# Kernel optimization log

Measured on AMD Instinct MI355X. Metric: run time of the kernel, lower is better.

## Reference

```python
import jax, jax.numpy as jnp
import numpy as np

B = 1024      # batch
HG = 28       # grid side (28x28 image -> graph)
N = HG * HG   # 784 nodes per sample
K = 70        # node_sampled (relaxed categorical classes)
GCN_OUT = 48
H_DIM = 400
Z = 70
IMG = 784
TEMP = 0.5


def _grid_edges():
    idx = np.arange(N).reshape(HG, HG)
    src = np.concatenate([idx[:, :-1].ravel(), idx[:, 1:].ravel(), idx[:-1, :].ravel(), idx[1:, :].ravel()])
    dst = np.concatenate([idx[:, 1:].ravel(), idx[:, :-1].ravel(), idx[1:, :].ravel(), idx[:-1, :].ravel()])
    loop = np.arange(N)
    return (np.concatenate([src, loop]).astype(np.int32),
            np.concatenate([dst, loop]).astype(np.int32))


def _lin(key, fi, fo):
    kw, kb = jax.random.split(key)
    s = 1.0 / np.sqrt(fi)
    return (jax.random.uniform(kw, (fi, fo), jnp.float32, -s, s),
            jax.random.uniform(kb, (fo,), jnp.float32, -s, s))


def setup_inputs() -> dict:
    key = jax.random.key(0)
    ks = jax.random.split(key, 16)
    src, dst = _grid_edges()
    u = jax.random.uniform(ks[2], (B, N, K), jnp.float32, 1e-6, 1.0 - 1e-6)
    inp = {
        'nodes': jax.random.normal(ks[0], (B, N, 2), jnp.float32),
        'logits': jax.random.normal(ks[1], (B, N, K), jnp.float32),
        'gumbel': -jnp.log(-jnp.log(u)),
        'eps': jax.random.normal(ks[3], (B, Z), jnp.float32),
    }
    inp['W1'], inp['b1'] = _lin(ks[4], 2, 16)
    inp['W2'], inp['b2'] = _lin(ks[5], 16, 32)
    inp['W3'], inp['b3'] = _lin(ks[6], 32, GCN_OUT)
    inp['We1'], inp['be1'] = _lin(ks[7], K * GCN_OUT, H_DIM)
    inp['We2'], inp['be2'] = _lin(ks[8], H_DIM, H_DIM)
    inp['Wmu'], inp['bmu'] = _lin(ks[9], H_DIM, Z)
    inp['Wvar'], inp['bvar'] = _lin(ks[10], H_DIM, Z)
    inp['Wd1'], inp['bd1'] = _lin(ks[11], Z, H_DIM)
    inp['Wd2'], inp['bd2'] = _lin(ks[12], H_DIM, IMG)
    inp['edge_src'] = jnp.asarray(src)
    inp['edge_dst'] = jnp.asarray(dst)
    return inp


def reference(nodes, logits, gumbel, eps,
              W1, b1, W2, b2, W3, b3,
              We1, be1, We2, be2,
              Wmu, bmu, Wvar, bvar,
              Wd1, bd1, Wd2, bd2,
              edge_src, edge_dst):
    # symmetric GCN normalization with self loops (already in edge list)
    deg = jnp.zeros((N,), nodes.dtype).at[edge_dst].add(1.0)
    dinv = jax.lax.rsqrt(deg)
    norm = dinv[edge_src] * dinv[edge_dst]  # [E]

    def gcn(h, W, b):
        h = h @ W                                   # [B,N,Fout]
        msg = h[:, edge_src] * norm[None, :, None]  # gather + scale, [B,E,Fout]
        return jnp.zeros_like(h).at[:, edge_dst].add(msg) + b

    h = jax.nn.relu(gcn(nodes, W1, b1))
    h = jax.nn.relu(gcn(h, W2, b2))
    h = jax.nn.relu(gcn(h, W3, b3))            # [B,N,48]

    # RelaxedOneHotCategorical(temp=0.5).rsample() == gumbel-softmax
    sample = jax.nn.softmax((logits + gumbel) / TEMP, axis=-1)  # [B,N,K]
    g = jnp.einsum('bnk,bnf->bkf', sample, h).reshape(h.shape[0], K * GCN_OUT)

    # encoder MLP + reparameterize
    e = jax.nn.relu(g @ We1 + be1)
    e = jax.nn.relu(e @ We2 + be2)
    mu = e @ Wmu + bmu
    var = jax.nn.softplus(e @ Wvar + bvar)
    z = mu + eps * jnp.sqrt(var + 1e-10)

    # decoder
    d = jax.nn.relu(z @ Wd1 + bd1)
    x_rec = jax.nn.sigmoid(d @ Wd2 + bd2)      # [B,784]
    return x_rec
```

## Files before the change

kernel.cpp:

```cpp
#include <hip/hip_runtime.h>
#include <hip/hip_bf16.h>


#define BB 1024
#define HG 28
#define NN 784
#define KK 70
#define F3 48
#define HD 400
#define ZD 70
#define IMGD 784

typedef __hip_bfloat16 bf16;
typedef __attribute__((ext_vector_type(8))) short s8v;
typedef __attribute__((ext_vector_type(4))) float f32x4;

__device__ __forceinline__ float dinv_ij(int i, int j){
  int deg = 1 + (i>0) + (i<HG-1) + (j>0) + (j<HG-1);
  return rsqrtf((float)deg);
}

__device__ __forceinline__ unsigned pk2(float a, float b){
  union { bf16 h; unsigned short u; } ua, ub;
  ua.h = __float2bfloat16(a); ub.h = __float2bfloat16(b);
  return ((unsigned)ub.u << 16) | ua.u;
}

__device__ __forceinline__ short bfbits(float v){
  union { bf16 h; short s; } u; u.h = __float2bfloat16(v); return u.s;
}

#define SYNC_LDS() do {                                   \
    asm volatile("" ::: "memory");                        \
    asm volatile("s_waitcnt lgkmcnt(0)" ::: "memory");    \
    __builtin_amdgcn_s_barrier();                         \
    asm volatile("" ::: "memory");                        \
  } while(0)

__global__ __launch_bounds__(256, 2)
void gcn_fused(const float* __restrict__ nodes,
               const float* __restrict__ W1, const float* __restrict__ b1,
               const float* __restrict__ W2, const float* __restrict__ b2,
               const float* __restrict__ W3, const float* __restrict__ b3,
               bf16* __restrict__ h3){
  __shared__ __align__(16) char smem[73216];
  float* regA = (float*)smem;
  float* regB = (float*)(smem + 36288);
  float* wbuf = (float*)(smem + 64512);
  float* W1s = wbuf;          float* b1s = wbuf + 32;
  float* W2s = wbuf + 48;     float* b2s = wbuf + 560;
  float* W3s = wbuf + 592;    float* b3s = wbuf + 2128;

  int tid = threadIdx.x;
  if (tid < 32)  W1s[tid] = W1[tid];
  if (tid < 16)  b1s[tid] = b1[tid];
  for (int t = tid; t < 512;  t += 256) W2s[t] = W2[t];
  if (tid < 32)  b2s[tid] = b2[tid];
  for (int t = tid; t < 1536; t += 256) W3s[t] = W3[t];
  if (tid < 48)  b3s[tid] = b3[tid];

  int b = blockIdx.x >> 2, s = blockIdx.x & 3;
  int base3 = s*7;
  int base2 = base3 - 1;
  int base1 = base3 - 2;
  const float* nb = nodes + (size_t)b*NN*2;
  __syncthreads();

  {
    float* h1s = regA;
    for (int t = tid; t < 308; t += 256){
      int lr = t/28, j = t - lr*28;
      int r = base1 + lr;
      float o[16] __attribute__((aligned(16)));
      if (r < 0 || r >= HG){
        #pragma unroll
        for (int f=0; f<16; f++) o[f] = 0.f;
      } else {
        float dn = dinv_ij(r,j);
        float a0 = dn*nb[(r*HG+j)*2+0], a1 = dn*nb[(r*HG+j)*2+1];
        if (r > 0)   { float w=dinv_ij(r-1,j); a0 += w*nb[((r-1)*HG+j)*2]; a1 += w*nb[((r-1)*HG+j)*2+1]; }
        if (r < HG-1){ float w=dinv_ij(r+1,j); a0 += w*nb[((r+1)*HG+j)*2]; a1 += w*nb[((r+1)*HG+j)*2+1]; }
        if (j > 0)   { float w=dinv_ij(r,j-1); a0 += w*nb[(r*HG+j-1)*2];   a1 += w*nb[(r*HG+j-1)*2+1]; }
        if (j < HG-1){ float w=dinv_ij(r,j+1); a0 += w*nb[(r*HG+j+1)*2];   a1 += w*nb[(r*HG+j+1)*2+1]; }
        a0 *= dn; a1 *= dn;
        #pragma unroll
        for (int f=0; f<16; f++) o[f] = fmaxf(a0*W1s[f] + a1*W1s[16+f] + b1s[f], 0.f);
      }
      float* dst = h1s + t*20;
      #pragma unroll
      for (int qq=0; qq<4; qq++) *(float4*)(dst + 4*qq) = *(float4*)&o[4*qq];
    }
  }
  __syncthreads();

  if (tid < 252){
    const float* h1s = regA;
    float* agg1 = regB;
    int lr = tid/28, j = tid - lr*28;
    int r = base2 + lr;
    float o[16] __attribute__((aligned(16)));
    if (r < 0 || r >= HG){
      #pragma unroll
      for (int f=0; f<16; f++) o[f] = 0.f;
    } else {
      int ln = (lr+1)*28 + j;
      float dn = dinv_ij(r,j);
      float wu = dinv_ij(r-1,j), wd = dinv_ij(r+1,j);
      float wl = (j>0)    ? dinv_ij(r,j-1) : 0.f;
      float wr = (j<HG-1) ? dinv_ij(r,j+1) : 0.f;
      const float* pc = h1s + ln*20;
      #pragma unroll
      for (int qq=0; qq<4; qq++){
        float4 vc = *(const float4*)(pc + 4*qq);
        float4 vu = *(const float4*)(pc - 28*20 + 4*qq);
        float4 vd = *(const float4*)(pc + 28*20 + 4*qq);
        float4 vl = *(const float4*)(pc - 20 + 4*qq);
        float4 vr = *(const float4*)(pc + 20 + 4*qq);
        o[4*qq+0] = dn*(dn*vc.x + wu*vu.x + wd*vd.x + wl*vl.x + wr*vr.x);
        o[4*qq+1] = dn*(dn*vc.y + wu*vu.y + wd*vd.y + wl*vl.y + wr*vr.y);
        o[4*qq+2] = dn*(dn*vc.z + wu*vu.z + wd*vd.z + wl*vl.z + wr*vr.z);
        o[4*qq+3] = dn*(dn*vc.w + wu*vu.w + wd*vd.w + wl*vl.w + wr*vr.w);
      }
    }
    float* dst = agg1 + tid*20;
    #pragma unroll
    for (int qq=0; qq<4; qq++) *(float4*)(dst + 4*qq) = *(float4*)&o[4*qq];
  }
  __syncthreads();

  {
    const float* agg1 = regB;
    float* h2s = regA;
    int tx = tid & 7, ty = tid >> 3;
    float4 w2r[16];
    #pragma unroll
    for (int fi=0; fi<16; fi++) w2r[fi] = *(const float4*)&W2s[fi*32 + tx*4];
    float4 bb = *(const float4*)&b2s[tx*4];
    #pragma unroll
    for (int i=0; i<8; i++){
      int n = ty + 32*i;
      if (n < 252){
        float af[16] __attribute__((aligned(16)));
        const float* ap = agg1 + n*20;
        #pragma unroll
        for (int qq=0; qq<4; qq++) *(float4*)&af[4*qq] = *(const float4*)(ap + 4*qq);
        float4 acc = bb;
        #pragma unroll
        for (int fi=0; fi<16; fi++){
          float a = af[fi];
          acc.x += a*w2r[fi].x; acc.y += a*w2r[fi].y;
          acc.z += a*w2r[fi].z; acc.w += a*w2r[fi].w;
        }
        acc.x = fmaxf(acc.x,0.f); acc.y = fmaxf(acc.y,0.f);
        acc.z = fmaxf(acc.z,0.f); acc.w = fmaxf(acc.w,0.f);
        *(float4*)&h2s[n*36 + tx*4] = acc;
      }
    }
  }
  __syncthreads();

  if (tid < 196){
    const float* h2s = regA;
    float* agg2 = regB;
    int lr = tid/28, j = tid - lr*28;
    int r = base3 + lr;
    int ln = (lr+1)*28 + j;
    float dn = dinv_ij(r,j);
    float wu = dinv_ij(r-1,j), wd = dinv_ij(r+1,j);
    float wl = (j>0)    ? dinv_ij(r,j-1) : 0.f;
    float wr = (j<HG-1) ? dinv_ij(r,j+1) : 0.f;
    const float* pc = h2s + ln*36;
    float* dst = agg2 + tid*36;
    #pragma unroll
    for (int qq=0; qq<8; qq++){
      float4 vc = *(const float4*)(pc + 4*qq);
      float4 vu = *(const float4*)(pc - 28*36 + 4*qq);
      float4 vd = *(const float4*)(pc + 28*36 + 4*qq);
      float4 vl = *(const float4*)(pc - 36 + 4*qq);
      float4 vr = *(const float4*)(pc + 36 + 4*qq);
      float4 o;
      o.x = dn*(dn*vc.x + wu*vu.x + wd*vd.x + wl*vl.x + wr*vr.x);
      o.y = dn*(dn*vc.y + wu*vu.y + wd*vd.y + wl*vl.y + wr*vr.y);
      o.z = dn*(dn*vc.z + wu*vu.z + wd*vd.z + wl*vl.z + wr*vr.z);
      o.w = dn*(dn*vc.w + wu*vu.w + wd*vd.w + wl*vl.w + wr*vr.w);
      *(float4*)(dst + 4*qq) = o;
    }
  }
  __syncthreads();

  {
    bf16* h3buf = (bf16*)regA;
    if (tid < 252){
      const float* agg2 = regB;
      int tx = tid % 12, ty = tid / 12;
      float4 w3r[32];
      #pragma unroll
      for (int fi=0; fi<32; fi++) w3r[fi] = *(const float4*)&W3s[fi*48 + tx*4];
      float4 bb = *(const float4*)&b3s[tx*4];
      #pragma unroll
      for (int i=0; i<10; i++){
        int n = ty + 21*i;
        if (n < 196){
          float af[32] __attribute__((aligned(16)));
          const float* ap = agg2 + n*36;
          #pragma unroll
          for (int qq=0; qq<8; qq++) *(float4*)&af[4*qq] = *(const float4*)(ap + 4*qq);
          float4 acc = bb;
          #pragma unroll
          for (int fi=0; fi<32; fi++){
            float a = af[fi];
            acc.x += a*w3r[fi].x; acc.y += a*w3r[fi].y;
            acc.z += a*w3r[fi].z; acc.w += a*w3r[fi].w;
          }
          uint2 pv;
          pv.x = pk2(fmaxf(acc.x,0.f), fmaxf(acc.y,0.f));
          pv.y = pk2(fmaxf(acc.z,0.f), fmaxf(acc.w,0.f));
          *(uint2*)((char*)h3buf + n*112 + tx*8) = pv;
        }
      }
    }
  }
  __syncthreads();

  {
    const char* h3buf = (const char*)regA;
    uint4* dst = (uint4*)(h3 + ((size_t)b*NN + base3*28)*F3);
    for (int t = tid; t < 1176; t += 256){
      int n = t/6, gq = t - n*6;
      dst[t] = *(const uint4*)(h3buf + n*112 + gq*16);
    }
  }
}

__global__
void einsum_mfma_kernel(const float* __restrict__ logits, const float* __restrict__ gumbel,
                        const bf16* __restrict__ h3, float* __restrict__ g){
  __shared__ __align__(16) unsigned smemS[7488];
  const int SLO = 2880, HTO = 5760;

  int b = blockIdx.x, tid = threadIdx.x;
  int l = tid & 63, w = tid >> 6;
  int n_loc = tid >> 2, q = tid & 3;
  int kstart = q << 4;
  int kcnt = (q < 3) ? 16 : 22;
  int kc2 = kcnt >> 1;
  int m_pair = tid >> 3;
  int half = (tid >> 2) & 1;
  int ks = w >> 1, mh = w & 1;
  int mtoff = mh ? 3 : 0, mtcnt = mh ? 2 : 3;

  for (int t = tid; t < 720; t += 256){
    int bb2 = t >= 360, r = t - bb2*360;
    if (bb2) smemS[SLO + 2520 + r] = 0u;
    else     smemS[2520 + r] = 0u;
  }

  f32x4 acc[3][3];
  #pragma unroll
  for (int mt=0; mt<3; mt++)
    #pragma unroll
    for (int bt=0; bt<3; bt++) acc[mt][bt] = (f32x4){0.f,0.f,0.f,0.f};

  int hm0 = tid/12, hj0 = tid - hm0*12;
  int tt1 = tid + 256;
  int hm1 = tt1/12, hj1 = tt1 - hm1*12;

  auto consume_pack = [&](int c){
    int c0 = c << 6;
    int node = c0 + n_loc;
    bool v = node < NN;
    const float* lp = logits + ((size_t)b*NN + node)*KK + kstart;
    const float* gp = gumbel + ((size_t)b*NN + node)*KK + kstart;
    int nld = (q < 3) ? 8 : 11;
    float x[22];
    #pragma unroll
    for (int s=0; s<11; s++){
      bool a = v && (s < nld);
      float2 lv = a ? *(const float2*)(lp + 2*s) : (float2){0.f,0.f};
      float2 gv = a ? *(const float2*)(gp + 2*s) : (float2){0.f,0.f};
      x[2*s]   = 2.f*(lv.x + gv.x);
      x[2*s+1] = 2.f*(lv.y + gv.y);
    }
    float mx = -1e30f;
    #pragma unroll
    for (int i=0; i<22; i++) if (i < kcnt) mx = fmaxf(mx, x[i]);
    mx = fmaxf(mx, __shfl_xor(mx, 1));
    mx = fmaxf(mx, __shfl_xor(mx, 2));
    float sum = 0.f;
    #pragma unroll
    for (int i=0; i<22; i++) if (i < kcnt){ x[i] = __expf(x[i]-mx); sum += x[i]; }
    sum += __shfl_xor(sum, 1);
    sum += __shfl_xor(sum, 2);
    float rs = v ? 1.0f/sum : 0.f;
    #pragma unroll
    for (int i=0; i<22; i++){
      if (i < kcnt){
        float p = x[i]*rs;
        unsigned hb = (unsigned)(unsigned short)bfbits(p);
        union { short s; bf16 h; } uh; uh.s = (short)hb;
        float lo = p - __bfloat162float(uh.h);
        unsigned lb = (unsigned)(unsigned short)bfbits(lo);
        unsigned phb = (unsigned)__shfl_xor((int)hb, 4);
        unsigned plb = (unsigned)__shfl_xor((int)lb, 4);
        unsigned dh = (half==0) ? (hb | (phb<<16)) : (phb | (hb<<16));
        unsigned dl = (half==0) ? (lb | (plb<<16)) : (plb | (lb<<16));
        bool doW = (half==0) ? (i < kc2) : (i >= kc2);
        if (doW){
          int k = kstart + i;
          int col = m_pair ^ (((k>>4)&3)<<3);
          smemS[k*36 + col] = dh;
          smemS[SLO + k*36 + col] = dl;
        }
      }
    }
    {
      bool vA0 = (c0 + 2*hm0)     < NN;
      bool vB0 = (c0 + 2*hm0 + 1) < NN;
      const uint2* p0 = (const uint2*)(h3 + ((size_t)b*NN + c0 + 2*hm0)*F3 + 4*hj0);
      uint2 hA0 = vA0 ? p0[0]  : (uint2){0u,0u};
      uint2 hB0 = vB0 ? p0[12] : (uint2){0u,0u};
      unsigned d0 = (hA0.x & 0xFFFFu) | (hB0.x << 16);
      unsigned d1 = (hA0.x >> 16)     | (hB0.x & 0xFFFF0000u);
      unsigned d2 = (hA0.y & 0xFFFFu) | (hB0.y << 16);
      unsigned d3 = (hA0.y >> 16)     | (hB0.y & 0xFFFF0000u);
      #pragma unroll
      for (int i2=0; i2<4; i2++){
        int f = 4*hj0 + i2;
        int col = hm0 ^ (((f>>4)&3)<<3);
        unsigned dv = (i2==0)?d0:(i2==1)?d1:(i2==2)?d2:d3;
        smemS[HTO + f*36 + col] = dv;
      }
      if (tid < 128){
        bool vA1 = (c0 + 2*hm1)     < NN;
        bool vB1 = (c0 + 2*hm1 + 1) < NN;
        const uint2* p1 = (const uint2*)(h3 + ((size_t)b*NN + c0 + 2*hm1)*F3 + 4*hj1);
        uint2 hA1 = vA1 ? p1[0]  : (uint2){0u,0u};
        uint2 hB1 = vB1 ? p1[12] : (uint2){0u,0u};
        unsigned e0 = (hA1.x & 0xFFFFu) | (hB1.x << 16);
        unsigned e1 = (hA1.x >> 16)     | (hB1.x & 0xFFFF0000u);
        unsigned e2 = (hA1.y & 0xFFFFu) | (hB1.y << 16);
        unsigned e3 = (hA1.y >> 16)     | (hB1.y & 0xFFFF0000u);
        #pragma unroll
        for (int i2=0; i2<4; i2++){
          int f = 4*hj1 + i2;
          int col = hm1 ^ (((f>>4)&3)<<3);
          unsigned dv = (i2==0)?e0:(i2==1)?e1:(i2==2)?e2:e3;
          smemS[HTO + f*36 + col] = dv;
        }
      }
    }
  };

  auto mfma_phase = [&](){
    int pr = (ks<<4) + ((l>>4)<<2);
    s8v Af[3], Al[3], Bf[3];
    #pragma unroll
    for (int mt=0; mt<3; mt++) if (mt < mtcnt){
      int row = (mtoff+mt)*16 + (l&15);
      int col = pr ^ (((row>>4)&3)<<3);
      Af[mt] = *(const s8v*)&smemS[row*36 + col];
      Al[mt] = *(const s8v*)&smemS[SLO + row*36 + col];
    }
    #pragma unroll
    for (int bt=0; bt<3; bt++){
      int f = bt*16 + (l&15);
      int col = pr ^ (((f>>4)&3)<<3);
      Bf[bt] = *(const s8v*)&smemS[HTO + f*36 + col];
    }
    #pragma unroll
    for (int mt=0; mt<3; mt++) if (mt < mtcnt)
      #pragma unroll
      for (int bt=0; bt<3; bt++){
        acc[mt][bt] = __builtin_amdgcn_mfma_f32_16x16x32_bf16(Af[mt], Bf[bt], acc[mt][bt], 0, 0, 0);
        acc[mt][bt] = __builtin_amdgcn_mfma_f32_16x16x32_bf16(Al[mt], Bf[bt], acc[mt][bt], 0, 0, 0);
      }
  };

  consume_pack(0);
  SYNC_LDS();

  for (int c = 0; c < 13; c++){
    mfma_phase();
    if (c < 12){
      SYNC_LDS();
      consume_pack(c+1);
      SYNC_LDS();
    }
  }

  __syncthreads();
  float* cred = (float*)&smemS[0];
  if (ks == 0){
    #pragma unroll
    for (int mt=0; mt<3; mt++) if (mt < mtcnt)
      #pragma unroll
      for (int bt=0; bt<3; bt++)
        #pragma unroll
        for (int r=0; r<4; r++){
          int row = (mtoff+mt)*16 + (l>>4)*4 + r;
          int col = bt*16 + (l&15);
          cred[row*49 + col] = acc[mt][bt][r];
        }
  }
  __syncthreads();
  if (ks == 1){
    #pragma unroll
    for (int mt=0; mt<3; mt++) if (mt < mtcnt)
      #pragma unroll
      for (int bt=0; bt<3; bt++)
        #pragma unroll
        for (int r=0; r<4; r++){
          int row = (mtoff+mt)*16 + (l>>4)*4 + r;
          int col = bt*16 + (l&15);
          cred[row*49 + col] += acc[mt][bt][r];
        }
  }
  __syncthreads();
  for (int t = tid; t < KK*F3; t += 256){
    int r = t / F3, c2 = t - r*F3;
    g[(size_t)b*(KK*F3) + t] = cred[r*49 + c2];
  }
}

template<int ACT>
__global__ __launch_bounds__(256)
void dense_kernel(const float* __restrict__ A, const float* __restrict__ W,
                  const float* __restrict__ bias, float* __restrict__ out,
                  int M, int K, int Nn, int kChunk){
  __shared__ float As[16][65];
  __shared__ float Bs[16][64];
  int tx = threadIdx.x & 15, ty = threadIdx.x >> 4;
  int m0 = blockIdx.x*64, n0 = blockIdx.y*64;
  int ks = blockIdx.z * kChunk;
  int ke = min(K, ks + kChunk);
  int a_kk = threadIdx.x & 15, a_mm = threadIdx.x >> 4;
  int b_nn = threadIdx.x & 63, b_k0 = threadIdx.x >> 6;
  float ra[4], rb[4];
  float acc[4][4] = {};

  #pragma unroll
  for (int s=0; s<4; s++){
    int gk = ks + a_kk;
    ra[s] = (gk < ke) ? A[(size_t)(m0 + a_mm + s*16)*K + gk] : 0.f;
  }
  #pragma unroll
  for (int s=0; s<4; s++){
    int gk = ks + b_k0 + s*4, gn = n0 + b_nn;
    rb[s] = (gk < ke && gn < Nn) ? W[(size_t)gk*Nn + gn] : 0.f;
  }

  for (int k0 = ks; k0 < ke; k0 += 16){
    #pragma unroll
    for (int s=0; s<4; s++) As[a_kk][a_mm + s*16] = ra[s];
    #pragma unroll
    for (int s=0; s<4; s++) Bs[b_k0 + s*4][b_nn] = rb[s];
    __syncthreads();
    if (k0 + 16 < ke){
      #pragma unroll
      for (int s=0; s<4; s++){
        int gk = k0 + 16 + a_kk;
        ra[s] = (gk < ke) ? A[(size_t)(m0 + a_mm + s*16)*K + gk] : 0.f;
      }
      #pragma unroll
      for (int s=0; s<4; s++){
        int gk = k0 + 16 + b_k0 + s*4, gn = n0 + b_nn;
        rb[s] = (gk < ke && gn < Nn) ? W[(size_t)gk*Nn + gn] : 0.f;
      }
    }
    #pragma unroll
    for (int kk=0; kk<16; kk++){
      float a[4], bv[4];
      #pragma unroll
      for (int i2=0; i2<4; i2++) a[i2] = As[kk][ty*4+i2];
      #pragma unroll
      for (int j2=0; j2<4; j2++) bv[j2] = Bs[kk][tx*4+j2];
      #pragma unroll
      for (int i2=0; i2<4; i2++)
        #pragma unroll
        for (int j2=0; j2<4; j2++) acc[i2][j2] += a[i2]*bv[j2];
    }
    __syncthreads();
  }

  if (ACT == 2){
    float* po = out + (size_t)blockIdx.z*M*Nn;
    #pragma unroll
    for (int j2=0; j2<4; j2++){
      int gn = n0 + tx*4 + j2;
      if (gn < Nn){
        #pragma unroll
        for (int i2=0; i2<4; i2++)
          po[(size_t)(m0 + ty*4 + i2)*Nn + gn] = acc[i2][j2];
      }
    }
  } else {
    #pragma unroll
    for (int j2=0; j2<4; j2++){
      int gn = n0 + tx*4 + j2;
      if (gn < Nn){
        float bb = bias[gn];
        #pragma unroll
        for (int i2=0; i2<4; i2++){
          float v = acc[i2][j2] + bb;
          v = (ACT == 0) ? fmaxf(v, 0.f) : 1.0f/(1.0f + __expf(-v));
          out[(size_t)(m0 + ty*4 + i2)*Nn + gn] = v;
        }
      }
    }
  }
}

__global__ __launch_bounds__(256)
void dense_dualB_partial(const float* __restrict__ A, const float* __restrict__ Wmu,
                         const float* __restrict__ Wvar, float* __restrict__ out,
                         int M, int K, int Nn, int kChunk){
  __shared__ float As[16][65];
  __shared__ float Bs[16][64];
  int tx = threadIdx.x & 15, ty = threadIdx.x >> 4;
  int m0 = blockIdx.x*64, n0 = blockIdx.y*64;
  int ks = blockIdx.z * kChunk;
  int ke = min(K, ks + kChunk);
  int a_kk = threadIdx.x & 15, a_mm = threadIdx.x >> 4;
  int b_nn = threadIdx.x & 63, b_k0 = threadIdx.x >> 6;
  float ra[4], rb[4];
  float acc[4][4] = {};

  auto bload = [&](int gk, int gn)->float{
    if (gk >= ke || gn >= Nn) return 0.f;
    return (gn < ZD) ? Wmu[(size_t)gk*ZD + gn] : Wvar[(size_t)gk*ZD + gn - ZD];
  };

  #pragma unroll
  for (int s=0; s<4; s++){
    int gk = ks + a_kk;
    ra[s] = (gk < ke) ? A[(size_t)(m0 + a_mm + s*16)*K + gk] : 0.f;
  }
  #pragma unroll
  for (int s=0; s<4; s++) rb[s] = bload(ks + b_k0 + s*4, n0 + b_nn);

  for (int k0 = ks; k0 < ke; k0 += 16){
    #pragma unroll
    for (int s=0; s<4; s++) As[a_kk][a_mm + s*16] = ra[s];
    #pragma unroll
    for (int s=0; s<4; s++) Bs[b_k0 + s*4][b_nn] = rb[s];
    __syncthreads();
    if (k0 + 16 < ke){
      #pragma unroll
      for (int s=0; s<4; s++){
        int gk = k0 + 16 + a_kk;
        ra[s] = (gk < ke) ? A[(size_t)(m0 + a_mm + s*16)*K + gk] : 0.f;
      }
      #pragma unroll
      for (int s=0; s<4; s++) rb[s] = bload(k0 + 16 + b_k0 + s*4, n0 + b_nn);
    }
    #pragma unroll
    for (int kk=0; kk<16; kk++){
      float a[4], bv[4];
      #pragma unroll
      for (int i2=0; i2<4; i2++) a[i2] = As[kk][ty*4+i2];
      #pragma unroll
      for (int j2=0; j2<4; j2++) bv[j2] = Bs[kk][tx*4+j2];
      #pragma unroll
      for (int i2=0; i2<4; i2++)
        #pragma unroll
        for (int j2=0; j2<4; j2++) acc[i2][j2] += a[i2]*bv[j2];
    }
    __syncthreads();
  }

  float* po = out + (size_t)blockIdx.z*M*Nn;
  #pragma unroll
  for (int j2=0; j2<4; j2++){
    int gn = n0 + tx*4 + j2;
    if (gn < Nn){
      #pragma unroll
      for (int i2=0; i2<4; i2++)
        po[(size_t)(m0 + ty*4 + i2)*Nn + gn] = acc[i2][j2];
    }
  }
}

template<int ACT>
__global__ __launch_bounds__(256)
void reduce_bias_act(const float* __restrict__ part, const float* __restrict__ bias,
                     float* __restrict__ out, int M, int Nn, int S){
  int idx = blockIdx.x*256 + threadIdx.x;
  if (idx >= M*Nn) return;
  int n = idx % Nn;
  float s = bias[n];
  for (int i=0; i<S; i++) s += part[(size_t)i*M*Nn + idx];
  out[idx] = (ACT == 0) ? fmaxf(s, 0.f) : 1.0f/(1.0f + __expf(-s));
}

__global__ __launch_bounds__(256)
void reduce_reparam(const float* __restrict__ part, const float* __restrict__ bmu,
                    const float* __restrict__ bvar, const float* __restrict__ eps,
                    float* __restrict__ z, int S){
  int idx = blockIdx.x*256 + threadIdx.x;
  int b = idx / ZD, zi = idx - b*ZD;
  float mu = bmu[zi], va = bvar[zi];
  for (int s=0; s<S; s++){
    const float* pr = part + ((size_t)s*BB + b)*140;
    mu += pr[zi];
    va += pr[ZD + zi];
  }
  float sp = fmaxf(va, 0.f) + log1pf(__expf(-fabsf(va)));
  z[idx] = mu + eps[idx]*sqrtf(sp + 1e-10f);
}

extern "C" void kernel_launch(void* const* d_in, const int* in_sizes, int n_in,
                              void* d_out, int out_size, void* d_ws, size_t ws_size,
                              hipStream_t stream){
  (void)in_sizes; (void)n_in; (void)out_size; (void)ws_size;
  const float* nodes  = (const float*)d_in[0];
  const float* logits = (const float*)d_in[1];
  const float* gumbel = (const float*)d_in[2];
  const float* eps    = (const float*)d_in[3];
  const float* W1 =(const float*)d_in[4],  *b1 =(const float*)d_in[5];
  const float* W2 =(const float*)d_in[6],  *b2 =(const float*)d_in[7];
  const float* W3 =(const float*)d_in[8],  *b3 =(const float*)d_in[9];
  const float* We1=(const float*)d_in[10], *be1=(const float*)d_in[11];
  const float* We2=(const float*)d_in[12], *be2=(const float*)d_in[13];
  const float* Wmu=(const float*)d_in[14], *bmu=(const float*)d_in[15];
  const float* Wvr=(const float*)d_in[16], *bvr=(const float*)d_in[17];
  const float* Wd1=(const float*)d_in[18], *bd1=(const float*)d_in[19];
  const float* Wd2=(const float*)d_in[20], *bd2=(const float*)d_in[21];

  char* ws = (char*)d_ws;
  bf16*  h3 = (bf16*)(ws);
  float* g  = (float*)(ws + 77070336);
  float* e1 = (float*)(ws + 90832896);
  float* e2 = (float*)(ws + 92471296);
  float* zb = (float*)(ws + 94109696);
  float* dd = (float*)(ws + 94396416);
  float* part = (float*)(ws);
  float* out = (float*)d_out;

  gcn_fused<<<4096, 256, 0, stream>>>(nodes, W1, b1, W2, b2, W3, b3, h3);
  einsum_mfma_kernel<<<1024, 256, 0, stream>>>(logits, gumbel, h3, g);
  dense_kernel<2><<<dim3(16, 7, 8), 256, 0, stream>>>(g, We1, nullptr, part, 1024, 3360, 400, 432);
  reduce_bias_act<0><<<1600, 256, 0, stream>>>(part, be1, e1, 1024, 400, 8);
  dense_kernel<2><<<dim3(16, 7, 4), 256, 0, stream>>>(e1, We2, nullptr, part, 1024, 400, 400, 112);
  reduce_bias_act<0><<<1600, 256, 0, stream>>>(part, be2, e2, 1024, 400, 4);
  dense_dualB_partial<<<dim3(16, 3, 4), 256, 0, stream>>>(e2, Wmu, Wvr, part, 1024, 400, 140, 112);
  reduce_reparam<<<280, 256, 0, stream>>>(part, bmu, bvr, eps, zb, 4);
  dense_kernel<0><<<dim3(16, 7, 1), 256, 0, stream>>>(zb, Wd1, bd1, dd, 1024, 70, 400, 70);
  dense_kernel<2><<<dim3(16, 13, 4), 256, 0, stream>>>(dd, Wd2, nullptr, part, 1024, 400, 784, 112);
  reduce_bias_act<1><<<3136, 256, 0, stream>>>(part, bd2, out, 1024, 784, 4);
}
```

Baseline: 400.9 us.

## Give each wave private node chunks in einsum kernel to drop block barriers

The einsum kernel is restructured so each of the four waves independently processes 32-node chunks (strided by wave), with its own private LDS staging for the softmax probabilities and h3 tiles. This removes the per-chunk block-wide barriers that previously separated softmax packing and MFMA phases. Each wave now covers all 80 rows of the K dimension (5 M-tiles), and a serial cross-wave reduction in LDS combines the partial results at the end. The trade-off is higher register use for accumulators, more LDS per block (which may lower occupancy), and less overlap within a wave between global loads and MFMA.

```diff
diff --git a/kernel.cpp b/kernel.cpp
--- a/kernel.cpp
+++ b/kernel.cpp
@@ -29,13 +29,6 @@
 __device__ __forceinline__ short bfbits(float v){
   union { bf16 h; short s; } u; u.h = __float2bfloat16(v); return u.s;
 }
-
-#define SYNC_LDS() do {                                   \
-    asm volatile("" ::: "memory");                        \
-    asm volatile("s_waitcnt lgkmcnt(0)" ::: "memory");    \
-    __builtin_amdgcn_s_barrier();                         \
-    asm volatile("" ::: "memory");                        \
-  } while(0)
 
 __global__ __launch_bounds__(256, 2)
 void gcn_fused(const float* __restrict__ nodes,
@@ -235,187 +228,152 @@
 __global__
 void einsum_mfma_kernel(const float* __restrict__ logits, const float* __restrict__ gumbel,
                         const bf16* __restrict__ h3, float* __restrict__ g){
-  __shared__ __align__(16) unsigned smemS[7488];
-  const int SLO = 2880, HTO = 5760;
+  __shared__ __align__(16) unsigned smemS[13312];
 
   int b = blockIdx.x, tid = threadIdx.x;
   int l = tid & 63, w = tid >> 6;
-  int n_loc = tid >> 2, q = tid & 3;
-  int kstart = q << 4;
-  int kcnt = (q < 3) ? 16 : 22;
-  int kc2 = kcnt >> 1;
-  int m_pair = tid >> 3;
-  int half = (tid >> 2) & 1;
-  int ks = w >> 1, mh = w & 1;
-  int mtoff = mh ? 3 : 0, mtcnt = mh ? 2 : 3;
-
-  for (int t = tid; t < 720; t += 256){
-    int bb2 = t >= 360, r = t - bb2*360;
-    if (bb2) smemS[SLO + 2520 + r] = 0u;
-    else     smemS[2520 + r] = 0u;
-  }
-
-  f32x4 acc[3][3];
+  unsigned* st  = smemS + w*3328;
+  unsigned* stl = st + 1280;
+  unsigned* ht  = st + 2560;
+
+  for (int t = l; t < 160; t += 64){ st[1120 + t] = 0u; stl[1120 + t] = 0u; }
+
+  f32x4 acc[5][3];
   #pragma unroll
-  for (int mt=0; mt<3; mt++)
+  for (int mt=0; mt<5; mt++)
     #pragma unroll
     for (int bt=0; bt<3; bt++) acc[mt][bt] = (f32x4){0.f,0.f,0.f,0.f};
 
-  int hm0 = tid/12, hj0 = tid - hm0*12;
-  int tt1 = tid + 256;
-  int hm1 = tt1/12, hj1 = tt1 - hm1*12;
-
-  auto consume_pack = [&](int c){
-    int c0 = c << 6;
-    int node = c0 + n_loc;
-    bool v = node < NN;
-    const float* lp = logits + ((size_t)b*NN + node)*KK + kstart;
-    const float* gp = gumbel + ((size_t)b*NN + node)*KK + kstart;
-    int nld = (q < 3) ? 8 : 11;
-    float x[22];
-    #pragma unroll
-    for (int s=0; s<11; s++){
-      bool a = v && (s < nld);
-      float2 lv = a ? *(const float2*)(lp + 2*s) : (float2){0.f,0.f};
-      float2 gv = a ? *(const float2*)(gp + 2*s) : (float2){0.f,0.f};
-      x[2*s]   = 2.f*(lv.x + gv.x);
-      x[2*s+1] = 2.f*(lv.y + gv.y);
+  int node_l = l >> 1;
+  int half = l & 1;
+  int pairm = l >> 2;
+  int nodehalf = (l >> 1) & 1;
+  int hm = l & 15, hq = l >> 4;
+
+  for (int c = w; c < 25; c += 4){
+    int c0 = c*32;
+    int n = c0 + node_l;
+    bool v = n < NN;
+    const float* lp = logits + ((size_t)b*NN + n)*KK;
+    const float* gp = gumbel + ((size_t)b*NN + n)*KK;
+    int kbase = half ? 34 : 0;
+    float x[35];
+    {
+      float2 lv[18], gv[18];
+      #pragma unroll
+      for (int s=0; s<18; s++){
+        lv[s] = v ? *(const float2*)(lp + kbase + 2*s) : (float2){0.f,0.f};
+        gv[s] = v ? *(const float2*)(gp + kbase + 2*s) : (float2){0.f,0.f};
+      }
+      if (half == 0){
+        #pragma unroll
+        for (int i=0; i<35; i++){
+          int s = i >> 1;
+          x[i] = (i & 1) ? 2.f*(lv[s].y + gv[s].y) : 2.f*(lv[s].x + gv[s].x);
+        }
+      } else {
+        x[0] = 2.f*(lv[0].y + gv[0].y);
+        #pragma unroll
+        for (int i=1; i<35; i++){
+          int s = (i + 1) >> 1;
+          x[i] = (i & 1) ? 2.f*(lv[s].x + gv[s].x) : 2.f*(lv[s].y + gv[s].y);
+        }
+      }
     }
     float mx = -1e30f;
     #pragma unroll
-    for (int i=0; i<22; i++) if (i < kcnt) mx = fmaxf(mx, x[i]);
+    for (int i=0; i<35; i++) mx = fmaxf(mx, x[i]);
     mx = fmaxf(mx, __shfl_xor(mx, 1));
-    mx = fmaxf(mx, __shfl_xor(mx, 2));
     float sum = 0.f;
     #pragma unroll
-    for (int i=0; i<22; i++) if (i < kcnt){ x[i] = __expf(x[i]-mx); sum += x[i]; }
+    for (int i=0; i<35; i++){ x[i] = __expf(x[i]-mx); sum += x[i]; }
     sum += __shfl_xor(sum, 1);
-    sum += __shfl_xor(sum, 2);
     float rs = v ? 1.0f/sum : 0.f;
     #pragma unroll
-    for (int i=0; i<22; i++){
-      if (i < kcnt){
-        float p = x[i]*rs;
-        unsigned hb = (unsigned)(unsigned short)bfbits(p);
-        union { short s; bf16 h; } uh; uh.s = (short)hb;
-        float lo = p - __bfloat162float(uh.h);
-        unsigned lb = (unsigned)(unsigned short)bfbits(lo);
-        unsigned phb = (unsigned)__shfl_xor((int)hb, 4);
-        unsigned plb = (unsigned)__shfl_xor((int)lb, 4);
-        unsigned dh = (half==0) ? (hb | (phb<<16)) : (phb | (hb<<16));
-        unsigned dl = (half==0) ? (lb | (plb<<16)) : (plb | (lb<<16));
-        bool doW = (half==0) ? (i < kc2) : (i >= kc2);
-        if (doW){
-          int k = kstart + i;
-          int col = m_pair ^ (((k>>4)&3)<<3);
-          smemS[k*36 + col] = dh;
-          smemS[SLO + k*36 + col] = dl;
+    for (int i=0; i<35; i++){
+      float p = x[i]*rs;
+      unsigned hb = (unsigned)(unsigned short)bfbits(p);
+      union { short s; bf16 h; } uh; uh.s = (short)hb;
+      float lo = p - __bfloat162float(uh.h);
+      unsigned lb = (unsigned)(unsigned short)bfbits(lo);
+      unsigned phb = (unsigned)__shfl_xor((int)hb, 2);
+      unsigned plb = (unsigned)__shfl_xor((int)lb, 2);
+      unsigned dh = (nodehalf==0) ? (hb | (phb<<16)) : (phb | (hb<<16));
+      unsigned dl = (nodehalf==0) ? (lb | (plb<<16)) : (plb | (lb<<16));
+      bool doW = (nodehalf==0) ? (i < 18) : (i >= 18);
+      if (doW){
+        int k = half*35 + i;
+        int grp = (pairm >> 2) ^ ((k >> 1) & 3);
+        int col = grp*4 + (pairm & 3);
+        st[k*16 + col] = dh;
+        stl[k*16 + col] = dl;
+      }
+    }
+    {
+      int nA = c0 + 2*hm, nB = nA + 1;
+      bool vA = nA < NN, vB = nB < NN;
+      const bf16* pA = h3 + ((size_t)b*NN + nA)*F3 + hq*12;
+      const bf16* pB = h3 + ((size_t)b*NN + nB)*F3 + hq*12;
+      #pragma unroll
+      for (int j=0; j<3; j++){
+        uint2 uA = vA ? *(const uint2*)(pA + 4*j) : (uint2){0u,0u};
+        uint2 uB = vB ? *(const uint2*)(pB + 4*j) : (uint2){0u,0u};
+        int f0 = hq*12 + 4*j;
+        unsigned dv[4];
+        dv[0] = (uA.x & 0xFFFFu) | (uB.x << 16);
+        dv[1] = (uA.x >> 16)     | (uB.x & 0xFFFF0000u);
+        dv[2] = (uA.y & 0xFFFFu) | (uB.y << 16);
+        dv[3] = (uA.y >> 16)     | (uB.y & 0xFFFF0000u);
+        #pragma unroll
+        for (int i2=0; i2<4; i2++){
+          int f = f0 + i2;
+          int grp = (hm >> 2) ^ ((f >> 1) & 3);
+          int col = grp*4 + (hm & 3);
+          ht[f*16 + col] = dv[i2];
         }
       }
     }
     {
-      bool vA0 = (c0 + 2*hm0)     < NN;
-      bool vB0 = (c0 + 2*hm0 + 1) < NN;
-      const uint2* p0 = (const uint2*)(h3 + ((size_t)b*NN + c0 + 2*hm0)*F3 + 4*hj0);
-      uint2 hA0 = vA0 ? p0[0]  : (uint2){0u,0u};
-      uint2 hB0 = vB0 ? p0[12] : (uint2){0u,0u};
-      unsigned d0 = (hA0.x & 0xFFFFu) | (hB0.x << 16);
-      unsigned d1 = (hA0.x >> 16)     | (hB0.x & 0xFFFF0000u);
-      unsigned d2 = (hA0.y & 0xFFFFu) | (hB0.y << 16);
-      unsigned d3 = (hA0.y >> 16)     | (hB0.y & 0xFFFF0000u);
-      #pragma unroll
-      for (int i2=0; i2<4; i2++){
-        int f = 4*hj0 + i2;
-        int col = hm0 ^ (((f>>4)&3)<<3);
-        unsigned dv = (i2==0)?d0:(i2==1)?d1:(i2==2)?d2:d3;
-        smemS[HTO + f*36 + col] = dv;
-      }
-      if (tid < 128){
-        bool vA1 = (c0 + 2*hm1)     < NN;
-        bool vB1 = (c0 + 2*hm1 + 1) < NN;
-        const uint2* p1 = (const uint2*)(h3 + ((size_t)b*NN + c0 + 2*hm1)*F3 + 4*hj1);
-        uint2 hA1 = vA1 ? p1[0]  : (uint2){0u,0u};
-        uint2 hB1 = vB1 ? p1[12] : (uint2){0u,0u};
-        unsigned e0 = (hA1.x & 0xFFFFu) | (hB1.x << 16);
-        unsigned e1 = (hA1.x >> 16)     | (hB1.x & 0xFFFF0000u);
-        unsigned e2 = (hA1.y & 0xFFFFu) | (hB1.y << 16);
-        unsigned e3 = (hA1.y >> 16)     | (hB1.y & 0xFFFF0000u);
-        #pragma unroll
-        for (int i2=0; i2<4; i2++){
-          int f = 4*hj1 + i2;
-          int col = hm1 ^ (((f>>4)&3)<<3);
-          unsigned dv = (i2==0)?e0:(i2==1)?e1:(i2==2)?e2:e3;
-          smemS[HTO + f*36 + col] = dv;
+      int lo4 = (l & 15) >> 1;
+      int grp = (l >> 4) ^ (lo4 & 3);
+      s8v Bf[3];
+      #pragma unroll
+      for (int bt=0; bt<3; bt++){
+        int fb = bt*16 + (l & 15);
+        Bf[bt] = *(const s8v*)&ht[fb*16 + grp*4];
+      }
+      #pragma unroll
+      for (int mt=0; mt<5; mt++){
+        int row = mt*16 + (l & 15);
+        s8v Af = *(const s8v*)&st[row*16 + grp*4];
+        s8v Al = *(const s8v*)&stl[row*16 + grp*4];
+        #pragma unroll
+        for (int bt=0; bt<3; bt++){
+          acc[mt][bt] = __builtin_amdgcn_mfma_f32_16x16x32_bf16(Af, Bf[bt], acc[mt][bt], 0, 0, 0);
+          acc[mt][bt] = __builtin_amdgcn_mfma_f32_16x16x32_bf16(Al, Bf[bt], acc[mt][bt], 0, 0, 0);
         }
       }
     }
-  };
-
-  auto mfma_phase = [&](){
-    int pr = (ks<<4) + ((l>>4)<<2);
-    s8v Af[3], Al[3], Bf[3];
-    #pragma unroll
-    for (int mt=0; mt<3; mt++) if (mt < mtcnt){
-      int row = (mtoff+mt)*16 + (l&15);
-      int col = pr ^ (((row>>4)&3)<<3);
-      Af[mt] = *(const s8v*)&smemS[row*36 + col];
-      Al[mt] = *(const s8v*)&smemS[SLO + row*36 + col];
-    }
-    #pragma unroll
-    for (int bt=0; bt<3; bt++){
-      int f = bt*16 + (l&15);
-      int col = pr ^ (((f>>4)&3)<<3);
-      Bf[bt] = *(const s8v*)&smemS[HTO + f*36 + col];
-    }
-    #pragma unroll
-    for (int mt=0; mt<3; mt++) if (mt < mtcnt)
-      #pragma unroll
-      for (int bt=0; bt<3; bt++){
-        acc[mt][bt] = __builtin_amdgcn_mfma_f32_16x16x32_bf16(Af[mt], Bf[bt], acc[mt][bt], 0, 0, 0);
-        acc[mt][bt] = __builtin_amdgcn_mfma_f32_16x16x32_bf16(Al[mt], Bf[bt], acc[mt][bt], 0, 0, 0);
-      }
-  };
-
-  consume_pack(0);
-  SYNC_LDS();
-
-  for (int c = 0; c < 13; c++){
-    mfma_phase();
-    if (c < 12){
-      SYNC_LDS();
-      consume_pack(c+1);
-      SYNC_LDS();
-    }
   }
 
   __syncthreads();
-  float* cred = (float*)&smemS[0];
-  if (ks == 0){
-    #pragma unroll
-    for (int mt=0; mt<3; mt++) if (mt < mtcnt)
-      #pragma unroll
-      for (int bt=0; bt<3; bt++)
-        #pragma unroll
-        for (int r=0; r<4; r++){
-          int row = (mtoff+mt)*16 + (l>>4)*4 + r;
-          int col = bt*16 + (l&15);
-          cred[row*49 + col] = acc[mt][bt][r];
-        }
-  }
-  __syncthreads();
-  if (ks == 1){
-    #pragma unroll
-    for (int mt=0; mt<3; mt++) if (mt < mtcnt)
-      #pragma unroll
-      for (int bt=0; bt<3; bt++)
-        #pragma unroll
-        for (int r=0; r<4; r++){
-          int row = (mtoff+mt)*16 + (l>>4)*4 + r;
-          int col = bt*16 + (l&15);
-          cred[row*49 + col] += acc[mt][bt][r];
-        }
-  }
-  __syncthreads();
+  float* cred = (float*)smemS;
+  for (int rw = 0; rw < 4; rw++){
+    if (w == rw){
+      #pragma unroll
+      for (int mt=0; mt<5; mt++)
+        #pragma unroll
+        for (int bt=0; bt<3; bt++)
+          #pragma unroll
+          for (int r=0; r<4; r++){
+            int row = mt*16 + (l>>4)*4 + r;
+            int col = bt*16 + (l&15);
+            if (rw == 0) cred[row*49 + col] = acc[mt][bt][r];
+            else         cred[row*49 + col] += acc[mt][bt][r];
+          }
+    }
+    __syncthreads();
+  }
   for (int t = tid; t < KK*F3; t += 256){
     int r = t / F3, c2 = t - r*F3;
     g[(size_t)b*(KK*F3) + t] = cred[r*49 + c2];
```

Measured after the change: 767.1 us. 1.91x slower.

## Fuse encoder tail GEMMs, reparameterization and decoder first layer into one kernel

Applied to the files above, without the earlier changes.

Replaces the We2 GEMM, its split-K reduction, the mu/var GEMM, reparameterization reduction and the Wd1 GEMM with a single kernel where each block processes four batch rows held in shared memory. This removes four launches and the partial-sum round trips through global memory. In exchange, weights are streamed directly from global/L2 by every block without tiling, so parallelism and reuse are much lower.

```diff
diff --git a/kernel.cpp b/kernel.cpp
--- a/kernel.cpp
+++ b/kernel.cpp
@@ -510,76 +510,6 @@
   }
 }
 
-__global__ __launch_bounds__(256)
-void dense_dualB_partial(const float* __restrict__ A, const float* __restrict__ Wmu,
-                         const float* __restrict__ Wvar, float* __restrict__ out,
-                         int M, int K, int Nn, int kChunk){
-  __shared__ float As[16][65];
-  __shared__ float Bs[16][64];
-  int tx = threadIdx.x & 15, ty = threadIdx.x >> 4;
-  int m0 = blockIdx.x*64, n0 = blockIdx.y*64;
-  int ks = blockIdx.z * kChunk;
-  int ke = min(K, ks + kChunk);
-  int a_kk = threadIdx.x & 15, a_mm = threadIdx.x >> 4;
-  int b_nn = threadIdx.x & 63, b_k0 = threadIdx.x >> 6;
-  float ra[4], rb[4];
-  float acc[4][4] = {};
-
-  auto bload = [&](int gk, int gn)->float{
-    if (gk >= ke || gn >= Nn) return 0.f;
-    return (gn < ZD) ? Wmu[(size_t)gk*ZD + gn] : Wvar[(size_t)gk*ZD + gn - ZD];
-  };
-
-  #pragma unroll
-  for (int s=0; s<4; s++){
-    int gk = ks + a_kk;
-    ra[s] = (gk < ke) ? A[(size_t)(m0 + a_mm + s*16)*K + gk] : 0.f;
-  }
-  #pragma unroll
-  for (int s=0; s<4; s++) rb[s] = bload(ks + b_k0 + s*4, n0 + b_nn);
-
-  for (int k0 = ks; k0 < ke; k0 += 16){
-    #pragma unroll
-    for (int s=0; s<4; s++) As[a_kk][a_mm + s*16] = ra[s];
-    #pragma unroll
-    for (int s=0; s<4; s++) Bs[b_k0 + s*4][b_nn] = rb[s];
-    __syncthreads();
-    if (k0 + 16 < ke){
-      #pragma unroll
-      for (int s=0; s<4; s++){
-        int gk = k0 + 16 + a_kk;
-        ra[s] = (gk < ke) ? A[(size_t)(m0 + a_mm + s*16)*K + gk] : 0.f;
-      }
-      #pragma unroll
-      for (int s=0; s<4; s++) rb[s] = bload(k0 + 16 + b_k0 + s*4, n0 + b_nn);
-    }
-    #pragma unroll
-    for (int kk=0; kk<16; kk++){
-      float a[4], bv[4];
-      #pragma unroll
-      for (int i2=0; i2<4; i2++) a[i2] = As[kk][ty*4+i2];
-      #pragma unroll
-      for (int j2=0; j2<4; j2++) bv[j2] = Bs[kk][tx*4+j2];
-      #pragma unroll
-      for (int i2=0; i2<4; i2++)
-        #pragma unroll
-        for (int j2=0; j2<4; j2++) acc[i2][j2] += a[i2]*bv[j2];
-    }
-    __syncthreads();
-  }
-
-  float* po = out + (size_t)blockIdx.z*M*Nn;
-  #pragma unroll
-  for (int j2=0; j2<4; j2++){
-    int gn = n0 + tx*4 + j2;
-    if (gn < Nn){
-      #pragma unroll
-      for (int i2=0; i2<4; i2++)
-        po[(size_t)(m0 + ty*4 + i2)*Nn + gn] = acc[i2][j2];
-    }
-  }
-}
-
 template<int ACT>
 __global__ __launch_bounds__(256)
 void reduce_bias_act(const float* __restrict__ part, const float* __restrict__ bias,
@@ -593,19 +523,56 @@
 }
 
 __global__ __launch_bounds__(256)
-void reduce_reparam(const float* __restrict__ part, const float* __restrict__ bmu,
-                    const float* __restrict__ bvar, const float* __restrict__ eps,
-                    float* __restrict__ z, int S){
-  int idx = blockIdx.x*256 + threadIdx.x;
-  int b = idx / ZD, zi = idx - b*ZD;
-  float mu = bmu[zi], va = bvar[zi];
-  for (int s=0; s<S; s++){
-    const float* pr = part + ((size_t)s*BB + b)*140;
-    mu += pr[zi];
-    va += pr[ZD + zi];
-  }
-  float sp = fmaxf(va, 0.f) + log1pf(__expf(-fabsf(va)));
-  z[idx] = mu + eps[idx]*sqrtf(sp + 1e-10f);
+void encoder_tail(const float* __restrict__ e1,
+                  const float* __restrict__ We2, const float* __restrict__ be2,
+                  const float* __restrict__ Wmu, const float* __restrict__ bmu,
+                  const float* __restrict__ Wvr, const float* __restrict__ bvr,
+                  const float* __restrict__ Wd1, const float* __restrict__ bd1,
+                  const float* __restrict__ eps, float* __restrict__ dd){
+  __shared__ float e1s[4][400];
+  __shared__ float e2s[4][400];
+  __shared__ float zs[4][72];
+  int tid = threadIdx.x;
+  int r0 = blockIdx.x * 4;
+  int col = tid & 63, row = tid >> 6;
+
+  for (int t = tid; t < 1600; t += 256)
+    e1s[t/400][t - (t/400)*400] = e1[(size_t)(r0 + t/400)*HD + (t - (t/400)*400)];
+  __syncthreads();
+
+  for (int n0 = 0; n0 < 400; n0 += 64){
+    int n = n0 + col;
+    if (n < 400){
+      float a = be2[n];
+      const float* er = e1s[row];
+      for (int k = 0; k < 400; k++) a += er[k] * We2[(size_t)k*HD + n];
+      e2s[row][n] = fmaxf(a, 0.f);
+    }
+  }
+  __syncthreads();
+
+  for (int zi = col; zi < ZD; zi += 64){
+    float amu = bmu[zi], avr = bvr[zi];
+    const float* er = e2s[row];
+    for (int k = 0; k < 400; k++){
+      float e = er[k];
+      amu += e * Wmu[(size_t)k*ZD + zi];
+      avr += e * Wvr[(size_t)k*ZD + zi];
+    }
+    float sp = fmaxf(avr, 0.f) + log1pf(__expf(-fabsf(avr)));
+    zs[row][zi] = amu + eps[(size_t)(r0 + row)*ZD + zi] * sqrtf(sp + 1e-10f);
+  }
+  __syncthreads();
+
+  for (int n0 = 0; n0 < 400; n0 += 64){
+    int n = n0 + col;
+    if (n < 400){
+      float a = bd1[n];
+      const float* zr = zs[row];
+      for (int k = 0; k < ZD; k++) a += zr[k] * Wd1[(size_t)k*HD + n];
+      dd[(size_t)(r0 + row)*HD + n] = fmaxf(a, 0.f);
+    }
+  }
 }
 
 extern "C" void kernel_launch(void* const* d_in, const int* in_sizes, int n_in,
@@ -630,8 +597,6 @@
   bf16*  h3 = (bf16*)(ws);
   float* g  = (float*)(ws + 77070336);
   float* e1 = (float*)(ws + 90832896);
-  float* e2 = (float*)(ws + 92471296);
-  float* zb = (float*)(ws + 94109696);
   float* dd = (float*)(ws + 94396416);
   float* part = (float*)(ws);
   float* out = (float*)d_out;
@@ -640,11 +605,7 @@
   einsum_mfma_kernel<<<1024, 256, 0, stream>>>(logits, gumbel, h3, g);
   dense_kernel<2><<<dim3(16, 7, 8), 256, 0, stream>>>(g, We1, nullptr, part, 1024, 3360, 400, 432);
   reduce_bias_act<0><<<1600, 256, 0, stream>>>(part, be1, e1, 1024, 400, 8);
-  dense_kernel<2><<<dim3(16, 7, 4), 256, 0, stream>>>(e1, We2, nullptr, part, 1024, 400, 400, 112);
-  reduce_bias_act<0><<<1600, 256, 0, stream>>>(part, be2, e2, 1024, 400, 4);
-  dense_dualB_partial<<<dim3(16, 3, 4), 256, 0, stream>>>(e2, Wmu, Wvr, part, 1024, 400, 140, 112);
-  reduce_reparam<<<280, 256, 0, stream>>>(part, bmu, bvr, eps, zb, 4);
-  dense_kernel<0><<<dim3(16, 7, 1), 256, 0, stream>>>(zb, Wd1, bd1, dd, 1024, 70, 400, 70);
+  encoder_tail<<<256, 256, 0, stream>>>(e1, We2, be2, Wmu, bmu, Wvr, bvr, Wd1, bd1, eps, dd);
   dense_kernel<2><<<dim3(16, 13, 4), 256, 0, stream>>>(dd, Wd2, nullptr, part, 1024, 400, 784, 112);
   reduce_bias_act<1><<<3136, 256, 0, stream>>>(part, bd2, out, 1024, 784, 4);
 }
```

Result: slower. 493.6 us (+23.1%).
